# Kernel optimization log

Hardware: AMD Instinct MI355X
Metric: run time of the kernel (lower is better)

Reference implementation:

```python
import jax, jax.numpy as jnp
import numpy as np

N = 50000
IN_DIM = 1024
HID = 64
HEADS = 4
OUT_DIM = 128
NEG_SLOPE = 0.2


def setup_inputs() -> dict:
    key = jax.random.key(0)
    ks = jax.random.split(key, 10)
    x = jax.random.normal(ks[0], (N, IN_DIM), dtype=jnp.float32)
    edge_index = jax.random.randint(ks[1], (2, 800000), 0, N, dtype=jnp.int64)
    # GATConv 1: input_dim -> hidden_dim, heads=HEADS, concat=True
    W1 = jax.random.normal(ks[2], (IN_DIM, HEADS * HID), dtype=jnp.float32) * (1.0 / np.sqrt(IN_DIM))
    att_src1 = jax.random.normal(ks[3], (HEADS, HID), dtype=jnp.float32) * 0.1
    att_dst1 = jax.random.normal(ks[4], (HEADS, HID), dtype=jnp.float32) * 0.1
    b1 = jnp.zeros((HEADS * HID,), dtype=jnp.float32)
    # GATConv 2: hidden_dim*heads -> output_dim, heads=1, concat=False
    W2 = jax.random.normal(ks[5], (HEADS * HID, OUT_DIM), dtype=jnp.float32) * (1.0 / np.sqrt(HEADS * HID))
    att_src2 = jax.random.normal(ks[6], (1, OUT_DIM), dtype=jnp.float32) * 0.1
    att_dst2 = jax.random.normal(ks[7], (1, OUT_DIM), dtype=jnp.float32) * 0.1
    b2 = jnp.zeros((OUT_DIM,), dtype=jnp.float32)
    return {"x": x, "edge_index": edge_index, "W1": W1, "att_src1": att_src1,
            "att_dst1": att_dst1, "b1": b1, "W2": W2, "att_src2": att_src2,
            "att_dst2": att_dst2, "b2": b2}


def _gat_conv(x, src, dst, W, a_src, a_dst, b, heads, concat):
    # x: [N, F_in]; src/dst: [E'] (self-loops already included)
    n = x.shape[0]
    h = (x @ W).reshape(n, heads, -1)                 # [N, H, D]
    # per-node attention halves (PyG style)
    alpha_s = jnp.sum(h * a_src[None], axis=-1)       # [N, H]
    alpha_d = jnp.sum(h * a_dst[None], axis=-1)       # [N, H]
    e = jax.nn.leaky_relu(alpha_s[src] + alpha_d[dst], NEG_SLOPE)  # [E', H]
    # segment softmax over incoming edges of each destination node
    m = jax.ops.segment_max(e, dst, num_segments=n)   # [N, H]
    m = jnp.where(jnp.isfinite(m), m, 0.0)
    e = jnp.exp(e - m[dst])
    s = jax.ops.segment_sum(e, dst, num_segments=n)   # [N, H]
    alpha = e / (s[dst] + 1e-16)                      # [E', H]
    out = jax.ops.segment_sum(h[src] * alpha[:, :, None], dst, num_segments=n)  # [N, H, D]
    out = out.reshape(n, -1) if concat else out.mean(axis=1)
    return out + b


def reference(x, edge_index, W1, att_src1, att_dst1, b1, W2, att_src2, att_dst2, b2):
    n = x.shape[0]
    # PyG GATConv default: add self-loops
    loops = jnp.arange(n, dtype=edge_index.dtype)
    src = jnp.concatenate([edge_index[0], loops])
    dst = jnp.concatenate([edge_index[1], loops])
    # dropout layers are identity in eval mode
    h = _gat_conv(x, src, dst, W1, att_src1, att_dst1, b1, HEADS, concat=True)
    h = jax.nn.elu(h)
    out = _gat_conv(h, src, dst, W2, att_src2, att_dst2, b2, 1, concat=False)
    # F.normalize(p=2, dim=-1)
    norm = jnp.maximum(jnp.linalg.norm(out, axis=-1, keepdims=True), 1e-12)
    return out / norm
```

## Files before the change

### kernel.cpp

```cpp
#include <hip/hip_runtime.h>
#include <math.h>

#define NNODES 50000
#define E0 800000
#define ETOT 850000
#define IN_DIM 1024
#define HEADS 4
#define C1 256
#define C2 128
#define NEG_SLOPE 0.2f

typedef short bf16x8 __attribute__((ext_vector_type(8)));
typedef float f32x4 __attribute__((ext_vector_type(4)));
typedef unsigned short ushort_t;

__device__ __forceinline__ void edge_sd(const int* __restrict__ ei, int e, int& s, int& d) {
    if (e < E0) { s = ei[e]; d = ei[E0 + e]; }
    else        { s = e - E0; d = s; }
}

__device__ __forceinline__ ushort_t f2b(float f) {
    unsigned u = __float_as_uint(f);
    return (ushort_t)((u + 0x7fffu + ((u >> 16) & 1u)) >> 16);
}
__device__ __forceinline__ float bf2f(ushort_t u) {
    return __uint_as_float((unsigned)u << 16);
}
__device__ __forceinline__ float lrelu(float v) { return v > 0.f ? v : NEG_SLOPE * v; }

__device__ __forceinline__ void gload_lds16(const void* g, void* l) {
    __builtin_amdgcn_global_load_lds(
        (const __attribute__((address_space(1))) unsigned int*)g,
        (__attribute__((address_space(3))) unsigned int*)l, 16, 0, 0);
}

__global__ __launch_bounds__(256) void wtrans_kernel(const float* __restrict__ W,
                                                     ushort_t* __restrict__ WT,
                                                     int K, int N)
{
    int idx = blockIdx.x * 256 + threadIdx.x;
    if (idx >= K * N) return;
    int k = idx / N, n = idx % N;
    WT[(size_t)n * K + k] = f2b(W[idx]);
}

__global__ __launch_bounds__(256, 6) void gemm_fb(const float* __restrict__ A,
                                                  const ushort_t* __restrict__ Bt,
                                                  ushort_t* __restrict__ Cb,
                                                  int M, int N, int K)
{
    __shared__ __align__(16) ushort_t As[2][4 * 64 * 8];
    __shared__ __align__(16) ushort_t Bs[2][4 * 128 * 8];

    const int tid  = threadIdx.x;
    const int lane = tid & 63;
    const int wid  = tid >> 6;
    const int wr   = wid >> 1, wc = wid & 1;
    const int rowBase = blockIdx.y * 64;
    const int colBase = blockIdx.x * 128;

    const int arow = tid >> 2;
    const int akc  = tid & 3;
    const int aGRow = min(rowBase + arow, M - 1);
    const float* aptr = A + (size_t)aGRow * K + akc * 8;
    const int awoff = akc * 512 + arow * 8;

    const ushort_t* bptr = Bt + (size_t)(colBase + lane) * K + wid * 8;
    const int bwoff0 = wid * 1024;
    const int bwoff1 = bwoff0 + 512;

    const int r0 = lane & 15;
    const int kh = lane >> 4;
    const int ardoff = kh * 512 + (wr * 32 + r0) * 8;
    const int brdoff = kh * 1024 + (wc * 64 + r0) * 8;

    f32x4 zero = {0.f, 0.f, 0.f, 0.f};
    f32x4 acc[2][4];
    #pragma unroll
    for (int i = 0; i < 2; ++i)
        #pragma unroll
        for (int j = 0; j < 4; ++j) acc[i][j] = zero;

    {
        float4 f0 = *(const float4*)(aptr + 0);
        float4 f1 = *(const float4*)(aptr + 4);
        bf16x8 p0;
        p0[0] = f2b(f0.x); p0[1] = f2b(f0.y); p0[2] = f2b(f0.z); p0[3] = f2b(f0.w);
        p0[4] = f2b(f1.x); p0[5] = f2b(f1.y); p0[6] = f2b(f1.z); p0[7] = f2b(f1.w);
        *(bf16x8*)&As[0][awoff] = p0;
        gload_lds16(bptr, &Bs[0][bwoff0]);
        gload_lds16(bptr + (size_t)64 * K, &Bs[0][bwoff1]);
    }
    __syncthreads();

    const ushort_t* rdA = As[0]; const ushort_t* rdB = Bs[0];
    ushort_t*       stA = As[1]; ushort_t*       stB = Bs[1];

    const int nt = K >> 5;
    for (int t = 0; t < nt; ++t) {
        const int kt = (t + 1) << 5;
        const bool has_next = kt < K;
        float4 f0, f1;
        if (has_next) {
            gload_lds16(bptr + kt, stB + bwoff0);
            gload_lds16(bptr + (size_t)64 * K + kt, stB + bwoff1);
            f0 = *(const float4*)(aptr + kt + 0);
            f1 = *(const float4*)(aptr + kt + 4);
        }

        bf16x8 af[2], bfr[4];
        #pragma unroll
        for (int fi = 0; fi < 2; ++fi) af[fi] = *(const bf16x8*)(rdA + ardoff + fi * 128);
        #pragma unroll
        for (int fj = 0; fj < 4; ++fj) bfr[fj] = *(const bf16x8*)(rdB + brdoff + fj * 128);
        #pragma unroll
        for (int fi = 0; fi < 2; ++fi)
            #pragma unroll
            for (int fj = 0; fj < 4; ++fj)
                acc[fi][fj] = __builtin_amdgcn_mfma_f32_16x16x32_bf16(
                    af[fi], bfr[fj], acc[fi][fj], 0, 0, 0);

        if (has_next) {
            bf16x8 p0;
            p0[0] = f2b(f0.x); p0[1] = f2b(f0.y); p0[2] = f2b(f0.z); p0[3] = f2b(f0.w);
            p0[4] = f2b(f1.x); p0[5] = f2b(f1.y); p0[6] = f2b(f1.z); p0[7] = f2b(f1.w);
            *(bf16x8*)(stA + awoff) = p0;
        }
        __syncthreads();
        const ushort_t* tA = rdA; rdA = stA; stA = (ushort_t*)tA;
        const ushort_t* tB = rdB; rdB = stB; stB = (ushort_t*)tB;
    }

    #pragma unroll
    for (int fi = 0; fi < 2; ++fi) {
        int row0 = rowBase + wr * 32 + fi * 16 + kh * 4;
        #pragma unroll
        for (int i = 0; i < 4; ++i) {
            int row = row0 + i;
            if (row < M) {
                #pragma unroll
                for (int fj = 0; fj < 4; ++fj)
                    Cb[(size_t)row * N + colBase + wc * 64 + fj * 16 + r0] = f2b(acc[fi][fj][i]);
            }
        }
    }
}

__global__ __launch_bounds__(256, 6) void gemm_bb(const ushort_t* __restrict__ Ab,
                                                  const ushort_t* __restrict__ Bt,
                                                  ushort_t* __restrict__ Cb,
                                                  int M, int N, int K)
{
    __shared__ __align__(16) ushort_t As[2][4 * 64 * 8];
    __shared__ __align__(16) ushort_t Bs[2][4 * 128 * 8];

    const int tid  = threadIdx.x;
    const int lane = tid & 63;
    const int wid  = tid >> 6;
    const int wr   = wid >> 1, wc = wid & 1;
    const int rowBase = blockIdx.y * 64;
    const int colBase = blockIdx.x * 128;

    const ushort_t* aptr = Ab + (size_t)min(rowBase + lane, M - 1) * K + wid * 8;
    const ushort_t* bptr = Bt + (size_t)(colBase + lane) * K + wid * 8;
    const int awoff  = wid * 512;
    const int bwoff0 = wid * 1024;
    const int bwoff1 = bwoff0 + 512;

    const int r0 = lane & 15;
    const int kh = lane >> 4;
    const int ardoff = kh * 512 + (wr * 32 + r0) * 8;
    const int brdoff = kh * 1024 + (wc * 64 + r0) * 8;

    f32x4 zero = {0.f, 0.f, 0.f, 0.f};
    f32x4 acc[2][4];
    #pragma unroll
    for (int i = 0; i < 2; ++i)
        #pragma unroll
        for (int j = 0; j < 4; ++j) acc[i][j] = zero;

    gload_lds16(aptr, &As[0][awoff]);
    gload_lds16(bptr, &Bs[0][bwoff0]);
    gload_lds16(bptr + (size_t)64 * K, &Bs[0][bwoff1]);
    __syncthreads();

    const ushort_t* rdA = As[0]; const ushort_t* rdB = Bs[0];
    ushort_t*       stA = As[1]; ushort_t*       stB = Bs[1];

    const int nt = K >> 5;
    for (int t = 0; t < nt; ++t) {
        const int kt = (t + 1) << 5;
        if (kt < K) {
            gload_lds16(aptr + kt, stA + awoff);
            gload_lds16(bptr + kt, stB + bwoff0);
            gload_lds16(bptr + (size_t)64 * K + kt, stB + bwoff1);
        }

        bf16x8 af[2], bfr[4];
        #pragma unroll
        for (int fi = 0; fi < 2; ++fi) af[fi] = *(const bf16x8*)(rdA + ardoff + fi * 128);
        #pragma unroll
        for (int fj = 0; fj < 4; ++fj) bfr[fj] = *(const bf16x8*)(rdB + brdoff + fj * 128);
        #pragma unroll
        for (int fi = 0; fi < 2; ++fi)
            #pragma unroll
            for (int fj = 0; fj < 4; ++fj)
                acc[fi][fj] = __builtin_amdgcn_mfma_f32_16x16x32_bf16(
                    af[fi], bfr[fj], acc[fi][fj], 0, 0, 0);

        __syncthreads();
        const ushort_t* tA = rdA; rdA = stA; stA = (ushort_t*)tA;
        const ushort_t* tB = rdB; rdB = stB; stB = (ushort_t*)tB;
    }

    #pragma unroll
    for (int fi = 0; fi < 2; ++fi) {
        int row0 = rowBase + wr * 32 + fi * 16 + kh * 4;
        #pragma unroll
        for (int i = 0; i < 4; ++i) {
            int row = row0 + i;
            if (row < M) {
                #pragma unroll
                for (int fj = 0; fj < 4; ++fj)
                    Cb[(size_t)row * N + colBase + wc * 64 + fj * 16 + r0] = f2b(acc[fi][fj][i]);
            }
        }
    }
}

__global__ __launch_bounds__(256) void alpha1_kernel(const ushort_t* __restrict__ h1b,
                                                     const float* __restrict__ asrc,
                                                     const float* __restrict__ adst,
                                                     float* __restrict__ out_s,
                                                     float* __restrict__ out_d)
{
    int n = blockIdx.x;
    int t = threadIdx.x;
    float h = bf2f(h1b[(size_t)n * C1 + t]);
    float s = h * asrc[t];
    float d = h * adst[t];
    #pragma unroll
    for (int off = 32; off > 0; off >>= 1) {
        s += __shfl_down(s, off);
        d += __shfl_down(d, off);
    }
    if ((t & 63) == 0) {
        out_s[n * HEADS + (t >> 6)] = s;
        out_d[n * HEADS + (t >> 6)] = d;
    }
}

__global__ __launch_bounds__(64) void alpha2_kernel(const ushort_t* __restrict__ h2b,
                                                    const float* __restrict__ asrc,
                                                    const float* __restrict__ adst,
                                                    float* __restrict__ out_s,
                                                    float* __restrict__ out_d)
{
    int n = blockIdx.x;
    int t = threadIdx.x;
    float a = bf2f(h2b[(size_t)n * C2 + t]);
    float b = bf2f(h2b[(size_t)n * C2 + t + 64]);
    float s = a * asrc[t] + b * asrc[t + 64];
    float d = a * adst[t] + b * adst[t + 64];
    #pragma unroll
    for (int off = 32; off > 0; off >>= 1) {
        s += __shfl_down(s, off);
        d += __shfl_down(d, off);
    }
    if (t == 0) { out_s[n] = s; out_d[n] = d; }
}

__global__ __launch_bounds__(256) void deg_kernel(const int* __restrict__ ei,
                                                  int* __restrict__ deg)
{
    int e = blockIdx.x * blockDim.x + threadIdx.x;
    if (e >= ETOT) return;
    int s, d; edge_sd(ei, e, s, d);
    atomicAdd(&deg[d], 1);
}

#define SCAN_T 1024
__global__ __launch_bounds__(SCAN_T) void scan_kernel(const int* __restrict__ deg,
                                                      int* __restrict__ rowptr)
{
    __shared__ int wsum[16];
    __shared__ int chunk_tot;
    __shared__ int carry_s;
    const int t = threadIdx.x, lane = t & 63, w = t >> 6;
    if (t == 0) carry_s = 0;
    __syncthreads();
    for (int base = 0; base < NNODES; base += SCAN_T * 4) {
        int idx = base + t * 4;
        int v0 = (idx + 0 < NNODES) ? deg[idx + 0] : 0;
        int v1 = (idx + 1 < NNODES) ? deg[idx + 1] : 0;
        int v2 = (idx + 2 < NNODES) ? deg[idx + 2] : 0;
        int v3 = (idx + 3 < NNODES) ? deg[idx + 3] : 0;
        int p0 = v0, p1 = p0 + v1, p2 = p1 + v2, p3 = p2 + v3;
        int incl = p3;
        #pragma unroll
        for (int off = 1; off < 64; off <<= 1) {
            int nb = __shfl_up(incl, off);
            if (lane >= off) incl += nb;
        }
        if (lane == 63) wsum[w] = incl;
        __syncthreads();
        if (w == 0 && lane < 16) {
            int ws = wsum[lane];
            int wincl = ws;
            #pragma unroll
            for (int off = 1; off < 16; off <<= 1) {
                int nb = __shfl_up(wincl, off);
                if (lane >= off) wincl += nb;
            }
            wsum[lane] = wincl - ws;
            if (lane == 15) chunk_tot = wincl;
        }
        __syncthreads();
        int carry = carry_s;
        int basev = carry + wsum[w] + (incl - p3);
        if (idx + 0 < NNODES) rowptr[idx + 0] = basev;
        if (idx + 1 < NNODES) rowptr[idx + 1] = basev + p0;
        if (idx + 2 < NNODES) rowptr[idx + 2] = basev + p1;
        if (idx + 3 < NNODES) rowptr[idx + 3] = basev + p2;
        __syncthreads();
        if (t == 0) carry_s = carry + chunk_tot;
        __syncthreads();
    }
    if (threadIdx.x == 0) rowptr[NNODES] = carry_s;
}

__global__ __launch_bounds__(256) void scatter_kernel(const int* __restrict__ ei,
                                                      int* __restrict__ cursor,
                                                      int* __restrict__ srcs)
{
    int e = blockIdx.x * blockDim.x + threadIdx.x;
    if (e >= ETOT) return;
    int s, d; edge_sd(ei, e, s, d);
    int pos = atomicAdd(&cursor[d], 1);
    srcs[pos] = s;
}

__global__ __launch_bounds__(256) void weights1_kernel(const int* __restrict__ rowptr,
                                                       const int* __restrict__ srcs,
                                                       const float4* __restrict__ as1,
                                                       const float4* __restrict__ ad1,
                                                       float4* __restrict__ wbuf)
{
    int d = blockIdx.x * 4 + (threadIdx.x >> 6);
    if (d >= NNODES) return;
    int lane = threadIdx.x & 63;
    int beg = rowptr[d], end = rowptr[d + 1];
    float4 adv = ad1[d];
    float m0 = -INFINITY, m1 = -INFINITY, m2 = -INFINITY, m3 = -INFINITY;
    for (int i = beg + lane; i < end; i += 64) {
        int s = srcs[i];
        float4 av = as1[s];
        m0 = fmaxf(m0, lrelu(av.x + adv.x));
        m1 = fmaxf(m1, lrelu(av.y + adv.y));
        m2 = fmaxf(m2, lrelu(av.z + adv.z));
        m3 = fmaxf(m3, lrelu(av.w + adv.w));
    }
    #pragma unroll
    for (int off = 32; off > 0; off >>= 1) {
        m0 = fmaxf(m0, __shfl_xor(m0, off));
        m1 = fmaxf(m1, __shfl_xor(m1, off));
        m2 = fmaxf(m2, __shfl_xor(m2, off));
        m3 = fmaxf(m3, __shfl_xor(m3, off));
    }
    float s0 = 0.f, s1 = 0.f, s2 = 0.f, s3 = 0.f;
    for (int i = beg + lane; i < end; i += 64) {
        int s = srcs[i];
        float4 av = as1[s];
        float w0 = expf(lrelu(av.x + adv.x) - m0);
        float w1 = expf(lrelu(av.y + adv.y) - m1);
        float w2 = expf(lrelu(av.z + adv.z) - m2);
        float w3 = expf(lrelu(av.w + adv.w) - m3);
        wbuf[i] = make_float4(w0, w1, w2, w3);
        s0 += w0; s1 += w1; s2 += w2; s3 += w3;
    }
    #pragma unroll
    for (int off = 32; off > 0; off >>= 1) {
        s0 += __shfl_xor(s0, off);
        s1 += __shfl_xor(s1, off);
        s2 += __shfl_xor(s2, off);
        s3 += __shfl_xor(s3, off);
    }
    float i0 = 1.f / (s0 + 1e-16f), i1 = 1.f / (s1 + 1e-16f);
    float i2 = 1.f / (s2 + 1e-16f), i3 = 1.f / (s3 + 1e-16f);
    for (int i = beg + lane; i < end; i += 64) {
        float4 wv = wbuf[i];
        wbuf[i] = make_float4(wv.x * i0, wv.y * i1, wv.z * i2, wv.w * i3);
    }
}

__global__ __launch_bounds__(256) void weights2_kernel(const int* __restrict__ rowptr,
                                                       const int* __restrict__ srcs,
                                                       const float* __restrict__ as2,
                                                       const float* __restrict__ ad2,
                                                       float* __restrict__ wbuf)
{
    int d = blockIdx.x * 4 + (threadIdx.x >> 6);
    if (d >= NNODES) return;
    int lane = threadIdx.x & 63;
    int beg = rowptr[d], end = rowptr[d + 1];
    float adv = ad2[d];
    float m = -INFINITY;
    for (int i = beg + lane; i < end; i += 64)
        m = fmaxf(m, lrelu(as2[srcs[i]] + adv));
    #pragma unroll
    for (int off = 32; off > 0; off >>= 1) m = fmaxf(m, __shfl_xor(m, off));
    float sm = 0.f;
    for (int i = beg + lane; i < end; i += 64) {
        float w = expf(lrelu(as2[srcs[i]] + adv) - m);
        wbuf[i] = w;
        sm += w;
    }
    #pragma unroll
    for (int off = 32; off > 0; off >>= 1) sm += __shfl_xor(sm, off);
    float inv = 1.f / (sm + 1e-16f);
    for (int i = beg + lane; i < end; i += 64) wbuf[i] *= inv;
}

__global__ __launch_bounds__(256) void aggr1_csr(const int* __restrict__ rowptr,
                                                 const int* __restrict__ srcs,
                                                 const ushort_t* __restrict__ h1b,
                                                 const float* __restrict__ wbuf,
                                                 const float* __restrict__ b1,
                                                 ushort_t* __restrict__ out)
{
    int d = blockIdx.x * 4 + (threadIdx.x >> 6);
    if (d >= NNODES) return;
    int lane = threadIdx.x & 63;
    int c0 = lane * 4;
    int head = lane >> 4;
    int beg = rowptr[d], end = rowptr[d + 1];
    float a0 = 0.f, a1 = 0.f, a2 = 0.f, a3 = 0.f;
    int i = beg;
    for (; i + 1 < end; i += 2) {
        int s0 = srcs[i], s1 = srcs[i + 1];
        float w0 = wbuf[i * 4 + head], w1 = wbuf[i * 4 + 4 + head];
        ushort4 v0 = *(const ushort4*)(h1b + (size_t)s0 * C1 + c0);
        ushort4 v1 = *(const ushort4*)(h1b + (size_t)s1 * C1 + c0);
        a0 = fmaf(w0, bf2f(v0.x), a0); a1 = fmaf(w0, bf2f(v0.y), a1);
        a2 = fmaf(w0, bf2f(v0.z), a2); a3 = fmaf(w0, bf2f(v0.w), a3);
        a0 = fmaf(w1, bf2f(v1.x), a0); a1 = fmaf(w1, bf2f(v1.y), a1);
        a2 = fmaf(w1, bf2f(v1.z), a2); a3 = fmaf(w1, bf2f(v1.w), a3);
    }
    if (i < end) {
        int s0 = srcs[i];
        float w0 = wbuf[i * 4 + head];
        ushort4 v0 = *(const ushort4*)(h1b + (size_t)s0 * C1 + c0);
        a0 = fmaf(w0, bf2f(v0.x), a0); a1 = fmaf(w0, bf2f(v0.y), a1);
        a2 = fmaf(w0, bf2f(v0.z), a2); a3 = fmaf(w0, bf2f(v0.w), a3);
    }
    float4 bv = *(const float4*)(b1 + c0);
    float o0 = a0 + bv.x, o1 = a1 + bv.y, o2 = a2 + bv.z, o3 = a3 + bv.w;
    ushort4 r;
    r.x = f2b(o0 > 0.f ? o0 : (expf(o0) - 1.f));
    r.y = f2b(o1 > 0.f ? o1 : (expf(o1) - 1.f));
    r.z = f2b(o2 > 0.f ? o2 : (expf(o2) - 1.f));
    r.w = f2b(o3 > 0.f ? o3 : (expf(o3) - 1.f));
    *(ushort4*)(out + (size_t)d * C1 + c0) = r;
}

__global__ __launch_bounds__(256) void aggr2_csr(const int* __restrict__ rowptr,
                                                 const int* __restrict__ srcs,
                                                 const ushort_t* __restrict__ h2b,
                                                 const float* __restrict__ wbuf,
                                                 const float* __restrict__ b2,
                                                 float* __restrict__ out)
{
    int d = blockIdx.x * 4 + (threadIdx.x >> 6);
    if (d >= NNODES) return;
    int lane = threadIdx.x & 63;
    int c0 = lane * 2;
    int beg = rowptr[d], end = rowptr[d + 1];
    float a0 = 0.f, a1 = 0.f;
    int i = beg;
    for (; i + 1 < end; i += 2) {
        int s0 = srcs[i], s1 = srcs[i + 1];
        float w0 = wbuf[i], w1 = wbuf[i + 1];
        ushort2 v0 = *(const ushort2*)(h2b + (size_t)s0 * C2 + c0);
        ushort2 v1 = *(const ushort2*)(h2b + (size_t)s1 * C2 + c0);
        a0 = fmaf(w0, bf2f(v0.x), a0); a1 = fmaf(w0, bf2f(v0.y), a1);
        a0 = fmaf(w1, bf2f(v1.x), a0); a1 = fmaf(w1, bf2f(v1.y), a1);
    }
    if (i < end) {
        float w0 = wbuf[i];
        ushort2 v0 = *(const ushort2*)(h2b + (size_t)srcs[i] * C2 + c0);
        a0 = fmaf(w0, bf2f(v0.x), a0); a1 = fmaf(w0, bf2f(v0.y), a1);
    }
    float2 bv = *(const float2*)(b2 + c0);
    float o0 = a0 + bv.x, o1 = a1 + bv.y;
    float sq = o0 * o0 + o1 * o1;
    #pragma unroll
    for (int off = 32; off > 0; off >>= 1) sq += __shfl_xor(sq, off);
    float inv = 1.0f / fmaxf(sqrtf(sq), 1e-12f);
    float2 r = make_float2(o0 * inv, o1 * inv);
    *(float2*)(out + (size_t)d * C2 + c0) = r;
}

extern "C" void kernel_launch(void* const* d_in, const int* in_sizes, int n_in,
                              void* d_out, int out_size, void* d_ws, size_t ws_size,
                              hipStream_t stream)
{
    const float* x     = (const float*)d_in[0];
    const int*   ei    = (const int*)d_in[1];
    const float* W1    = (const float*)d_in[2];
    const float* asrc1 = (const float*)d_in[3];
    const float* adst1 = (const float*)d_in[4];
    const float* b1    = (const float*)d_in[5];
    const float* W2    = (const float*)d_in[6];
    const float* asrc2 = (const float*)d_in[7];
    const float* adst2 = (const float*)d_in[8];
    const float* b2    = (const float*)d_in[9];
    float* out = (float*)d_out;

    char* ws = (char*)d_ws;
    size_t off = 0;
    auto alloc = [&](size_t nbytes) {
        void* p = ws + off;
        off += (nbytes + 15) & ~(size_t)15;
        return p;
    };
    ushort_t* h1b    = (ushort_t*)alloc((size_t)NNODES * C1 * 2);
    ushort_t* act1b  = (ushort_t*)alloc((size_t)NNODES * C1 * 2);
    ushort_t* h2b    = (ushort_t*)alloc((size_t)NNODES * C2 * 2);
    ushort_t* W1T    = (ushort_t*)alloc((size_t)C1 * IN_DIM * 2);
    ushort_t* W2T    = (ushort_t*)alloc((size_t)C2 * C1 * 2);
    float*    as1    = (float*)alloc((size_t)NNODES * HEADS * 4);
    float*    ad1    = (float*)alloc((size_t)NNODES * HEADS * 4);
    float*    as2    = (float*)alloc((size_t)NNODES * 4);
    float*    ad2    = (float*)alloc((size_t)NNODES * 4);
    float*    wbuf1  = (float*)alloc((size_t)ETOT * HEADS * 4);
    float*    wbuf2  = (float*)alloc((size_t)ETOT * 4);
    int*      deg    = (int*)alloc((size_t)NNODES * 4);
    int*      rowptr = (int*)alloc((size_t)(NNODES + 1) * 4);
    int*      cursor = (int*)alloc((size_t)(NNODES + 1) * 4);
    int*      srcs   = (int*)alloc((size_t)ETOT * 4);

    const int eb = (ETOT + 255) / 256;
    const int nb4 = (NNODES + 3) / 4;

    wtrans_kernel<<<(IN_DIM * C1 + 255) / 256, 256, 0, stream>>>(W1, W1T, IN_DIM, C1);
    wtrans_kernel<<<(C1 * C2 + 255) / 256, 256, 0, stream>>>(W2, W2T, C1, C2);

    hipMemsetAsync(deg, 0, (size_t)NNODES * 4, stream);
    deg_kernel<<<eb, 256, 0, stream>>>(ei, deg);
    scan_kernel<<<1, SCAN_T, 0, stream>>>(deg, rowptr);
    hipMemcpyAsync(cursor, rowptr, (size_t)(NNODES + 1) * 4, hipMemcpyDeviceToDevice, stream);
    scatter_kernel<<<eb, 256, 0, stream>>>(ei, cursor, srcs);

    dim3 g1(C1 / 128, (NNODES + 63) / 64);
    gemm_fb<<<g1, 256, 0, stream>>>(x, W1T, h1b, NNODES, C1, IN_DIM);
    alpha1_kernel<<<NNODES, 256, 0, stream>>>(h1b, asrc1, adst1, as1, ad1);
    weights1_kernel<<<nb4, 256, 0, stream>>>(rowptr, srcs, (const float4*)as1,
                                             (const float4*)ad1, (float4*)wbuf1);
    aggr1_csr<<<nb4, 256, 0, stream>>>(rowptr, srcs, h1b, wbuf1, b1, act1b);

    dim3 g2(C2 / 128, (NNODES + 63) / 64);
    gemm_bb<<<g2, 256, 0, stream>>>(act1b, W2T, h2b, NNODES, C2, C1);
    alpha2_kernel<<<NNODES, 64, 0, stream>>>(h2b, asrc2, adst2, as2, ad2);
    weights2_kernel<<<nb4, 256, 0, stream>>>(rowptr, srcs, as2, ad2, wbuf2);
    aggr2_csr<<<nb4, 256, 0, stream>>>(rowptr, srcs, h2b, wbuf2, b2, out);
}
```

Measured before the change: 489.6 us.

## Load GEMM A fragments directly to registers, block-interleave weights, double K step

The two GEMMs no longer stage the A operand through LDS. Each lane loads its MFMA A fragment straight from global memory into registers, converting to bf16 in the fp32 case. The weight matrix is now pre-transposed into a k-blocked-by-8 layout, so B tiles of 64 K-values load contiguously into LDS, and each loop iteration covers 64 K instead of 32. This halves barrier count and removes the LDS write and read round trip for A. In exchange, the uncoalesced row-wise A global loads and the larger LDS and register footprint may lower occupancy (launch bound drops from 6 to 4).

```diff
diff --git a/kernel.cpp b/kernel.cpp
--- a/kernel.cpp
+++ b/kernel.cpp
@@ -34,6 +34,13 @@
         (__attribute__((address_space(3))) unsigned int*)l, 16, 0, 0);
 }
 
+__device__ __forceinline__ bf16x8 cvt_bf8(float4 f0, float4 f1) {
+    bf16x8 p;
+    p[0] = f2b(f0.x); p[1] = f2b(f0.y); p[2] = f2b(f0.z); p[3] = f2b(f0.w);
+    p[4] = f2b(f1.x); p[5] = f2b(f1.y); p[6] = f2b(f1.z); p[7] = f2b(f1.w);
+    return p;
+}
+
 __global__ __launch_bounds__(256) void wtrans_kernel(const float* __restrict__ W,
                                                      ushort_t* __restrict__ WT,
                                                      int K, int N)
@@ -41,16 +48,15 @@
     int idx = blockIdx.x * 256 + threadIdx.x;
     if (idx >= K * N) return;
     int k = idx / N, n = idx % N;
-    WT[(size_t)n * K + k] = f2b(W[idx]);
-}
-
-__global__ __launch_bounds__(256, 6) void gemm_fb(const float* __restrict__ A,
-                                                  const ushort_t* __restrict__ Bt,
+    WT[((size_t)(k >> 3) * N + n) * 8 + (k & 7)] = f2b(W[idx]);
+}
+
+__global__ __launch_bounds__(256, 4) void gemm_fb(const float* __restrict__ A,
+                                                  const ushort_t* __restrict__ Bblk,
                                                   ushort_t* __restrict__ Cb,
                                                   int M, int N, int K)
 {
-    __shared__ __align__(16) ushort_t As[2][4 * 64 * 8];
-    __shared__ __align__(16) ushort_t Bs[2][4 * 128 * 8];
+    __shared__ __align__(16) ushort_t Bs[2][8 * 128 * 8];
 
     const int tid  = threadIdx.x;
     const int lane = tid & 63;
@@ -58,21 +64,20 @@
     const int wr   = wid >> 1, wc = wid & 1;
     const int rowBase = blockIdx.y * 64;
     const int colBase = blockIdx.x * 128;
-
-    const int arow = tid >> 2;
-    const int akc  = tid & 3;
-    const int aGRow = min(rowBase + arow, M - 1);
-    const float* aptr = A + (size_t)aGRow * K + akc * 8;
-    const int awoff = akc * 512 + arow * 8;
-
-    const ushort_t* bptr = Bt + (size_t)(colBase + lane) * K + wid * 8;
-    const int bwoff0 = wid * 1024;
-    const int bwoff1 = bwoff0 + 512;
-
     const int r0 = lane & 15;
     const int kh = lane >> 4;
-    const int ardoff = kh * 512 + (wr * 32 + r0) * 8;
-    const int brdoff = kh * 1024 + (wc * 64 + r0) * 8;
+
+    const float* aP0 = A + (size_t)min(rowBase + wr * 32 + r0,      M - 1) * K + kh * 8;
+    const float* aP1 = A + (size_t)min(rowBase + wr * 32 + 16 + r0, M - 1) * K + kh * 8;
+
+    const int p0 = wid * 2;
+    const ushort_t* bsrc0 = Bblk + ((size_t)(p0 + 0) * N + colBase + lane) * 8;
+    const ushort_t* bsrc1 = Bblk + ((size_t)(p0 + 1) * N + colBase + lane) * 8;
+    const int bdst0 = (p0 + 0) * 1024;
+    const int bdst1 = (p0 + 1) * 1024;
+    const size_t bstep = (size_t)8 * N * 8;
+
+    const int brd = (wc * 64 + r0) * 8;
 
     f32x4 zero = {0.f, 0.f, 0.f, 0.f};
     f32x4 acc[2][4];
@@ -81,54 +86,60 @@
         #pragma unroll
         for (int j = 0; j < 4; ++j) acc[i][j] = zero;
 
-    {
-        float4 f0 = *(const float4*)(aptr + 0);
-        float4 f1 = *(const float4*)(aptr + 4);
-        bf16x8 p0;
-        p0[0] = f2b(f0.x); p0[1] = f2b(f0.y); p0[2] = f2b(f0.z); p0[3] = f2b(f0.w);
-        p0[4] = f2b(f1.x); p0[5] = f2b(f1.y); p0[6] = f2b(f1.z); p0[7] = f2b(f1.w);
-        *(bf16x8*)&As[0][awoff] = p0;
-        gload_lds16(bptr, &Bs[0][bwoff0]);
-        gload_lds16(bptr + (size_t)64 * K, &Bs[0][bwoff1]);
-    }
+    gload_lds16(bsrc0,       &Bs[0][bdst0]);
+    gload_lds16(bsrc0 + 512, &Bs[0][bdst0 + 512]);
+    gload_lds16(bsrc1,       &Bs[0][bdst1]);
+    gload_lds16(bsrc1 + 512, &Bs[0][bdst1 + 512]);
+    float4 n00 = *(const float4*)(aP0 +  0), n01 = *(const float4*)(aP0 +  4);
+    float4 n02 = *(const float4*)(aP0 + 32), n03 = *(const float4*)(aP0 + 36);
+    float4 n10 = *(const float4*)(aP1 +  0), n11 = *(const float4*)(aP1 +  4);
+    float4 n12 = *(const float4*)(aP1 + 32), n13 = *(const float4*)(aP1 + 36);
     __syncthreads();
 
-    const ushort_t* rdA = As[0]; const ushort_t* rdB = Bs[0];
-    ushort_t*       stA = As[1]; ushort_t*       stB = Bs[1];
-
-    const int nt = K >> 5;
+    const ushort_t* rdB = Bs[0];
+    ushort_t*       stB = Bs[1];
+
+    bf16x8 aC[2][2];
+    aC[0][0] = cvt_bf8(n00, n01); aC[0][1] = cvt_bf8(n02, n03);
+    aC[1][0] = cvt_bf8(n10, n11); aC[1][1] = cvt_bf8(n12, n13);
+
+    const int nt = K >> 6;
     for (int t = 0; t < nt; ++t) {
-        const int kt = (t + 1) << 5;
+        const int kt = (t + 1) << 6;
         const bool has_next = kt < K;
-        float4 f0, f1;
         if (has_next) {
-            gload_lds16(bptr + kt, stB + bwoff0);
-            gload_lds16(bptr + (size_t)64 * K + kt, stB + bwoff1);
-            f0 = *(const float4*)(aptr + kt + 0);
-            f1 = *(const float4*)(aptr + kt + 4);
-        }
-
-        bf16x8 af[2], bfr[4];
-        #pragma unroll
-        for (int fi = 0; fi < 2; ++fi) af[fi] = *(const bf16x8*)(rdA + ardoff + fi * 128);
-        #pragma unroll
-        for (int fj = 0; fj < 4; ++fj) bfr[fj] = *(const bf16x8*)(rdB + brdoff + fj * 128);
-        #pragma unroll
-        for (int fi = 0; fi < 2; ++fi)
+            const ushort_t* b0 = bsrc0 + (size_t)(t + 1) * bstep;
+            const ushort_t* b1 = bsrc1 + (size_t)(t + 1) * bstep;
+            gload_lds16(b0,       stB + bdst0);
+            gload_lds16(b0 + 512, stB + bdst0 + 512);
+            gload_lds16(b1,       stB + bdst1);
+            gload_lds16(b1 + 512, stB + bdst1 + 512);
+            n00 = *(const float4*)(aP0 + kt +  0); n01 = *(const float4*)(aP0 + kt +  4);
+            n02 = *(const float4*)(aP0 + kt + 32); n03 = *(const float4*)(aP0 + kt + 36);
+            n10 = *(const float4*)(aP1 + kt +  0); n11 = *(const float4*)(aP1 + kt +  4);
+            n12 = *(const float4*)(aP1 + kt + 32); n13 = *(const float4*)(aP1 + kt + 36);
+        }
+
+        #pragma unroll
+        for (int kc = 0; kc < 2; ++kc) {
+            const ushort_t* bbase = rdB + (kc * 4 + kh) * 1024 + brd;
+            bf16x8 bF[4];
             #pragma unroll
-            for (int fj = 0; fj < 4; ++fj)
-                acc[fi][fj] = __builtin_amdgcn_mfma_f32_16x16x32_bf16(
-                    af[fi], bfr[fj], acc[fi][fj], 0, 0, 0);
+            for (int fj = 0; fj < 4; ++fj) bF[fj] = *(const bf16x8*)(bbase + fj * 128);
+            #pragma unroll
+            for (int fi = 0; fi < 2; ++fi)
+                #pragma unroll
+                for (int fj = 0; fj < 4; ++fj)
+                    acc[fi][fj] = __builtin_amdgcn_mfma_f32_16x16x32_bf16(
+                        aC[fi][kc], bF[fj], acc[fi][fj], 0, 0, 0);
+        }
 
         if (has_next) {
-            bf16x8 p0;
-            p0[0] = f2b(f0.x); p0[1] = f2b(f0.y); p0[2] = f2b(f0.z); p0[3] = f2b(f0.w);
-            p0[4] = f2b(f1.x); p0[5] = f2b(f1.y); p0[6] = f2b(f1.z); p0[7] = f2b(f1.w);
-            *(bf16x8*)(stA + awoff) = p0;
+            aC[0][0] = cvt_bf8(n00, n01); aC[0][1] = cvt_bf8(n02, n03);
+            aC[1][0] = cvt_bf8(n10, n11); aC[1][1] = cvt_bf8(n12, n13);
         }
         __syncthreads();
-        const ushort_t* tA = rdA; rdA = stA; stA = (ushort_t*)tA;
-        const ushort_t* tB = rdB; rdB = stB; stB = (ushort_t*)tB;
+        ushort_t* tmp = (ushort_t*)rdB; rdB = stB; stB = tmp;
     }
 
     #pragma unroll
@@ -146,13 +157,12 @@
     }
 }
 
-__global__ __launch_bounds__(256, 6) void gemm_bb(const ushort_t* __restrict__ Ab,
-                                                  const ushort_t* __restrict__ Bt,
+__global__ __launch_bounds__(256, 4) void gemm_bb(const ushort_t* __restrict__ Ab,
+                                                  const ushort_t* __restrict__ Bblk,
                                                   ushort_t* __restrict__ Cb,
                                                   int M, int N, int K)
 {
-    __shared__ __align__(16) ushort_t As[2][4 * 64 * 8];
-    __shared__ __align__(16) ushort_t Bs[2][4 * 128 * 8];
+    __shared__ __align__(16) ushort_t Bs[2][8 * 128 * 8];
 
     const int tid  = threadIdx.x;
     const int lane = tid & 63;
@@ -160,17 +170,20 @@
     const int wr   = wid >> 1, wc = wid & 1;
     const int rowBase = blockIdx.y * 64;
     const int colBase = blockIdx.x * 128;
-
-    const ushort_t* aptr = Ab + (size_t)min(rowBase + lane, M - 1) * K + wid * 8;
-    const ushort_t* bptr = Bt + (size_t)(colBase + lane) * K + wid * 8;
-    const int awoff  = wid * 512;
-    const int bwoff0 = wid * 1024;
-    const int bwoff1 = bwoff0 + 512;
-
     const int r0 = lane & 15;
     const int kh = lane >> 4;
-    const int ardoff = kh * 512 + (wr * 32 + r0) * 8;
-    const int brdoff = kh * 1024 + (wc * 64 + r0) * 8;
+
+    const ushort_t* aP0 = Ab + (size_t)min(rowBase + wr * 32 + r0,      M - 1) * K + kh * 8;
+    const ushort_t* aP1 = Ab + (size_t)min(rowBase + wr * 32 + 16 + r0, M - 1) * K + kh * 8;
+
+    const int p0 = wid * 2;
+    const ushort_t* bsrc0 = Bblk + ((size_t)(p0 + 0) * N + colBase + lane) * 8;
+    const ushort_t* bsrc1 = Bblk + ((size_t)(p0 + 1) * N + colBase + lane) * 8;
+    const int bdst0 = (p0 + 0) * 1024;
+    const int bdst1 = (p0 + 1) * 1024;
+    const size_t bstep = (size_t)8 * N * 8;
+
+    const int brd = (wc * 64 + r0) * 8;
 
     f32x4 zero = {0.f, 0.f, 0.f, 0.f};
     f32x4 acc[2][4];
@@ -179,38 +192,53 @@
         #pragma unroll
         for (int j = 0; j < 4; ++j) acc[i][j] = zero;
 
-    gload_lds16(aptr, &As[0][awoff]);
-    gload_lds16(bptr, &Bs[0][bwoff0]);
-    gload_lds16(bptr + (size_t)64 * K, &Bs[0][bwoff1]);
+    gload_lds16(bsrc0,       &Bs[0][bdst0]);
+    gload_lds16(bsrc0 + 512, &Bs[0][bdst0 + 512]);
+    gload_lds16(bsrc1,       &Bs[0][bdst1]);
+    gload_lds16(bsrc1 + 512, &Bs[0][bdst1 + 512]);
+    bf16x8 aC[2][2], aN[2][2];
+    aC[0][0] = *(const bf16x8*)(aP0 +  0); aC[0][1] = *(const bf16x8*)(aP0 + 32);
+    aC[1][0] = *(const bf16x8*)(aP1 +  0); aC[1][1] = *(const bf16x8*)(aP1 + 32);
     __syncthreads();
 
-    const ushort_t* rdA = As[0]; const ushort_t* rdB = Bs[0];
-    ushort_t*       stA = As[1]; ushort_t*       stB = Bs[1];
-
-    const int nt = K >> 5;
+    const ushort_t* rdB = Bs[0];
+    ushort_t*       stB = Bs[1];
+
+    const int nt = K >> 6;
     for (int t = 0; t < nt; ++t) {
-        const int kt = (t + 1) << 5;
-        if (kt < K) {
-            gload_lds16(aptr + kt, stA + awoff);
-            gload_lds16(bptr + kt, stB + bwoff0);
-            gload_lds16(bptr + (size_t)64 * K + kt, stB + bwoff1);
-        }
-
-        bf16x8 af[2], bfr[4];
-        #pragma unroll
-        for (int fi = 0; fi < 2; ++fi) af[fi] = *(const bf16x8*)(rdA + ardoff + fi * 128);
-        #pragma unroll
-        for (int fj = 0; fj < 4; ++fj) bfr[fj] = *(const bf16x8*)(rdB + brdoff + fj * 128);
-        #pragma unroll
-        for (int fi = 0; fi < 2; ++fi)
+        const int kt = (t + 1) << 6;
+        const bool has_next = kt < K;
+        if (has_next) {
+            const ushort_t* b0 = bsrc0 + (size_t)(t + 1) * bstep;
+            const ushort_t* b1 = bsrc1 + (size_t)(t + 1) * bstep;
+            gload_lds16(b0,       stB + bdst0);
+            gload_lds16(b0 + 512, stB + bdst0 + 512);
+            gload_lds16(b1,       stB + bdst1);
+            gload_lds16(b1 + 512, stB + bdst1 + 512);
+            aN[0][0] = *(const bf16x8*)(aP0 + kt +  0); aN[0][1] = *(const bf16x8*)(aP0 + kt + 32);
+            aN[1][0] = *(const bf16x8*)(aP1 + kt +  0); aN[1][1] = *(const bf16x8*)(aP1 + kt + 32);
+        }
+
+        #pragma unroll
+        for (int kc = 0; kc < 2; ++kc) {
+            const ushort_t* bbase = rdB + (kc * 4 + kh) * 1024 + brd;
+            bf16x8 bF[4];
             #pragma unroll
-            for (int fj = 0; fj < 4; ++fj)
-                acc[fi][fj] = __builtin_amdgcn_mfma_f32_16x16x32_bf16(
-                    af[fi], bfr[fj], acc[fi][fj], 0, 0, 0);
-
+            for (int fj = 0; fj < 4; ++fj) bF[fj] = *(const bf16x8*)(bbase + fj * 128);
+            #pragma unroll
+            for (int fi = 0; fi < 2; ++fi)
+                #pragma unroll
+                for (int fj = 0; fj < 4; ++fj)
+                    acc[fi][fj] = __builtin_amdgcn_mfma_f32_16x16x32_bf16(
+                        aC[fi][kc], bF[fj], acc[fi][fj], 0, 0, 0);
+        }
+
+        if (has_next) {
+            aC[0][0] = aN[0][0]; aC[0][1] = aN[0][1];
+            aC[1][0] = aN[1][0]; aC[1][1] = aN[1][1];
+        }
         __syncthreads();
-        const ushort_t* tA = rdA; rdA = stA; stA = (ushort_t*)tA;
-        const ushort_t* tB = rdB; rdB = stB; stB = (ushort_t*)tB;
+        ushort_t* tmp = (ushort_t*)rdB; rdB = stB; stB = tmp;
     }
 
     #pragma unroll
@@ -526,8 +554,8 @@
     ushort_t* h1b    = (ushort_t*)alloc((size_t)NNODES * C1 * 2);
     ushort_t* act1b  = (ushort_t*)alloc((size_t)NNODES * C1 * 2);
     ushort_t* h2b    = (ushort_t*)alloc((size_t)NNODES * C2 * 2);
-    ushort_t* W1T    = (ushort_t*)alloc((size_t)C1 * IN_DIM * 2);
-    ushort_t* W2T    = (ushort_t*)alloc((size_t)C2 * C1 * 2);
+    ushort_t* W1blk  = (ushort_t*)alloc((size_t)C1 * IN_DIM * 2);
+    ushort_t* W2blk  = (ushort_t*)alloc((size_t)C2 * C1 * 2);
     float*    as1    = (float*)alloc((size_t)NNODES * HEADS * 4);
     float*    ad1    = (float*)alloc((size_t)NNODES * HEADS * 4);
     float*    as2    = (float*)alloc((size_t)NNODES * 4);
@@ -542,8 +570,8 @@
     const int eb = (ETOT + 255) / 256;
     const int nb4 = (NNODES + 3) / 4;
 
-    wtrans_kernel<<<(IN_DIM * C1 + 255) / 256, 256, 0, stream>>>(W1, W1T, IN_DIM, C1);
-    wtrans_kernel<<<(C1 * C2 + 255) / 256, 256, 0, stream>>>(W2, W2T, C1, C2);
+    wtrans_kernel<<<(IN_DIM * C1 + 255) / 256, 256, 0, stream>>>(W1, W1blk, IN_DIM, C1);
+    wtrans_kernel<<<(C1 * C2 + 255) / 256, 256, 0, stream>>>(W2, W2blk, C1, C2);
 
     hipMemsetAsync(deg, 0, (size_t)NNODES * 4, stream);
     deg_kernel<<<eb, 256, 0, stream>>>(ei, deg);
@@ -552,14 +580,14 @@
     scatter_kernel<<<eb, 256, 0, stream>>>(ei, cursor, srcs);
 
     dim3 g1(C1 / 128, (NNODES + 63) / 64);
-    gemm_fb<<<g1, 256, 0, stream>>>(x, W1T, h1b, NNODES, C1, IN_DIM);
+    gemm_fb<<<g1, 256, 0, stream>>>(x, W1blk, h1b, NNODES, C1, IN_DIM);
     alpha1_kernel<<<NNODES, 256, 0, stream>>>(h1b, asrc1, adst1, as1, ad1);
     weights1_kernel<<<nb4, 256, 0, stream>>>(rowptr, srcs, (const float4*)as1,
                                              (const float4*)ad1, (float4*)wbuf1);
     aggr1_csr<<<nb4, 256, 0, stream>>>(rowptr, srcs, h1b, wbuf1, b1, act1b);
 
     dim3 g2(C2 / 128, (NNODES + 63) / 64);
-    gemm_bb<<<g2, 256, 0, stream>>>(act1b, W2T, h2b, NNODES, C2, C1);
+    gemm_bb<<<g2, 256, 0, stream>>>(act1b, W2blk, h2b, NNODES, C2, C1);
     alpha2_kernel<<<NNODES, 64, 0, stream>>>(h2b, asrc2, adst2, as2, ad2);
     weights2_kernel<<<nb4, 256, 0, stream>>>(rowptr, srcs, as2, ad2, wbuf2);
     aggr2_csr<<<nb4, 256, 0, stream>>>(rowptr, srcs, h2b, wbuf2, b2, out);
```

Measured after the change: 491.4 us. Within noise of the previous version (+0.4%).
